# Performance work log

Measured on AMD Instinct MI355X. Metric: run time of the kernel, lower is better.

The kernel has to match this reference:

```python
import jax, jax.numpy as jnp
import numpy as np

EPS = 1e-5  # torch LayerNorm default


def _layer_norm(x, g, b):
    mu = jnp.mean(x, axis=-1, keepdims=True)
    var = jnp.mean(jnp.square(x - mu), axis=-1, keepdims=True)
    return (x - mu) * jax.lax.rsqrt(var + EPS) * g + b


def setup_inputs() -> dict:
    key = jax.random.key(0)
    ks = jax.random.split(key, 8)
    B, S, D = 4, 2048, 1024
    s = 1.0 / np.sqrt(D)
    return {
        "q": jax.random.normal(ks[0], (B, S, D), jnp.float32),
        "k": jax.random.normal(ks[1], (B, S, D), jnp.float32),
        "v": jax.random.normal(ks[2], (B, S, D), jnp.float32),
        "mask": jnp.ones((B, 1, S), jnp.int32),
        "Wq": jax.random.normal(ks[3], (D, D), jnp.float32) * s,
        "Wk": jax.random.normal(ks[4], (D, D), jnp.float32) * s,
        "Wv": jax.random.normal(ks[5], (D, D), jnp.float32) * s,
        "Wo": jax.random.normal(ks[6], (D, D), jnp.float32) * s,
        "ln_q_g": jnp.ones((D,), jnp.float32),
        "ln_q_b": jnp.zeros((D,), jnp.float32),
        "ln_k_g": jnp.ones((D,), jnp.float32),
        "ln_k_b": jnp.zeros((D,), jnp.float32),
        "ln_v_g": jnp.ones((D,), jnp.float32),
        "ln_v_b": jnp.zeros((D,), jnp.float32),
    }


def reference(q, k, v, mask, Wq, Wk, Wv, Wo,
              ln_q_g, ln_q_b, ln_k_g, ln_k_b, ln_v_g, ln_v_b):
    B, Lq, D = q.shape
    H = 16
    dk = D // H
    residual = q
    # pre-LN + bias-free projections
    qh = (_layer_norm(q, ln_q_g, ln_q_b) @ Wq).reshape(B, Lq, H, dk).transpose(0, 2, 1, 3)
    kh = (_layer_norm(k, ln_k_g, ln_k_b) @ Wk).reshape(B, -1, H, dk).transpose(0, 2, 1, 3)
    vh = (_layer_norm(v, ln_v_g, ln_v_b) @ Wv).reshape(B, -1, H, dk).transpose(0, 2, 1, 3)
    # scaled scores [B,H,Lq,Lk]
    scores = jnp.einsum('bhqd,bhkd->bhqk', qh, kh) / jnp.sqrt(jnp.float32(dk))
    pad = (mask == 0)[:, None, :, :]  # [B,1,*,Lk], True where masked
    scores = jnp.where(pad, -jnp.inf, scores)
    attn = jax.nn.softmax(scores, axis=-1)
    attn = jnp.where(pad, 0.0, attn)
    out = jnp.einsum('bhqk,bhkd->bhqd', attn, vh)
    out = out.transpose(0, 2, 1, 3).reshape(B, Lq, D)
    return out @ Wo + residual
```

## Files before the change

kernel.cpp:

```cpp
#include <hip/hip_runtime.h>
#include <stdint.h>

typedef __attribute__((ext_vector_type(8))) short short8;
typedef __attribute__((ext_vector_type(4))) float f32x4;
typedef __attribute__((ext_vector_type(4))) unsigned short us4;

#define B_ 4
#define S_ 2048
#define D_ 1024
#define H_ 16
#define DK_ 64

__device__ __forceinline__ unsigned short f2bf(float f) {
  union { float f; unsigned int u; } c; c.f = f;
  unsigned int r = (c.u + 0x7fffu + ((c.u >> 16) & 1u)) >> 16;
  return (unsigned short)r;
}

__device__ __forceinline__ unsigned int cvt_pk_bf16(float lo, float hi) {
  unsigned int r;
  asm("v_cvt_pk_bf16_f32 %0, %1, %2" : "=v"(r) : "v"(lo), "v"(hi));
  return r;
}

__device__ __forceinline__ float exp2_fast(float x) {
#if __has_builtin(__builtin_amdgcn_exp2f)
  return __builtin_amdgcn_exp2f(x);
#else
  float r; asm("v_exp_f32 %0, %1" : "=v"(r) : "v"(x)); return r;
#endif
}

__device__ __forceinline__ void glds16(const void* g, void* l) {
  __builtin_amdgcn_global_load_lds(
      (__attribute__((address_space(1))) void*)(uintptr_t)g,
      (__attribute__((address_space(3))) void*)l, 16, 0, 0);
}

__device__ __forceinline__ f32x4 mfma_bf16(short8 a, short8 b, f32x4 c) {
  return __builtin_amdgcn_mfma_f32_16x16x32_bf16(a, b, c, 0, 0, 0);
}

__global__ __launch_bounds__(256) void ln_bf16_3(const float* __restrict__ x0,
                                                 const float* __restrict__ x1,
                                                 const float* __restrict__ x2,
                                                 const float* __restrict__ g0,
                                                 const float* __restrict__ g1,
                                                 const float* __restrict__ g2,
                                                 const float* __restrict__ b0,
                                                 const float* __restrict__ b1,
                                                 const float* __restrict__ b2,
                                                 unsigned short* __restrict__ y0,
                                                 unsigned short* __restrict__ y1,
                                                 unsigned short* __restrict__ y2) {
  const int which = blockIdx.y;
  const float* x = which == 0 ? x0 : (which == 1 ? x1 : x2);
  const float* g = which == 0 ? g0 : (which == 1 ? g1 : g2);
  const float* bta = which == 0 ? b0 : (which == 1 ? b1 : b2);
  unsigned short* y = which == 0 ? y0 : (which == 1 ? y1 : y2);

  const int lane = threadIdx.x & 63, wid = threadIdx.x >> 6;
  const int row = blockIdx.x * 4 + wid;
  const float4* xr = (const float4*)(x + (size_t)row * D_);
  float4 v[4];
  float s1 = 0.f, s2 = 0.f;
#pragma unroll
  for (int i = 0; i < 4; ++i) {
    v[i] = xr[i * 64 + lane];
    s1 += v[i].x + v[i].y + v[i].z + v[i].w;
    s2 += v[i].x * v[i].x + v[i].y * v[i].y + v[i].z * v[i].z + v[i].w * v[i].w;
  }
#pragma unroll
  for (int m = 32; m; m >>= 1) { s1 += __shfl_xor(s1, m); s2 += __shfl_xor(s2, m); }
  const float mu = s1 * (1.f / D_);
  const float inv = rsqrtf(s2 * (1.f / D_) - mu * mu + 1e-5f);
  const float4* gp = (const float4*)g;
  const float4* bp = (const float4*)bta;
  us4* yr = (us4*)(y + (size_t)row * D_);
#pragma unroll
  for (int i = 0; i < 4; ++i) {
    float4 gv = gp[i * 64 + lane], bv = bp[i * 64 + lane];
    us4 o;
    o[0] = f2bf((v[i].x - mu) * inv * gv.x + bv.x);
    o[1] = f2bf((v[i].y - mu) * inv * gv.y + bv.y);
    o[2] = f2bf((v[i].z - mu) * inv * gv.z + bv.z);
    o[3] = f2bf((v[i].w - mu) * inv * gv.w + bv.w);
    yr[i * 64 + lane] = o;
  }
}

__global__ void wt_bf16_4(const float* __restrict__ W0, const float* __restrict__ W1,
                          const float* __restrict__ W2, const float* __restrict__ W3,
                          unsigned short* __restrict__ T0, unsigned short* __restrict__ T1,
                          unsigned short* __restrict__ T2, unsigned short* __restrict__ T3) {
  const int which = blockIdx.z;
  const float* W = which == 0 ? W0 : (which == 1 ? W1 : (which == 2 ? W2 : W3));
  unsigned short* Wt = which == 0 ? T0 : (which == 1 ? T1 : (which == 2 ? T2 : T3));
  __shared__ float t[32][33];
  const int n0 = blockIdx.x * 32, k0 = blockIdx.y * 32;
  const int tx = threadIdx.x, ty = threadIdx.y;
  for (int i = ty; i < 32; i += 8) t[i][tx] = W[(size_t)(k0 + i) * D_ + n0 + tx];
  __syncthreads();
  for (int i = ty; i < 32; i += 8)
    Wt[(size_t)(n0 + i) * D_ + k0 + tx] = f2bf(t[tx][i]);
}

__global__ __launch_bounds__(256, 2) void gemm_qkv(const unsigned short* __restrict__ Xq,
                                                   const unsigned short* __restrict__ Xk,
                                                   const unsigned short* __restrict__ Xv,
                                                   const unsigned short* __restrict__ Wq,
                                                   const unsigned short* __restrict__ Wk,
                                                   const unsigned short* __restrict__ Wv,
                                                   unsigned short* __restrict__ Qh,
                                                   unsigned short* __restrict__ Kh,
                                                   unsigned short* __restrict__ Vtb,
                                                   float qscale) {
  constexpr int K = D_;
  constexpr int NT = K / 64;
  __shared__ __attribute__((aligned(16))) unsigned short As[2][128][64];
  __shared__ __attribute__((aligned(16))) unsigned short Bs[2][128][64];
  const int z = blockIdx.z;
  const unsigned short* A = z == 0 ? Xq : (z == 1 ? Xk : Xv);
  const unsigned short* Bt = z == 0 ? Wq : (z == 1 ? Wk : Wv);
  const int tid = threadIdx.x;
  const int lane = tid & 63, wid = tid >> 6;
  const int lo16 = lane & 15, hi4 = lane >> 4;
  const int wr = wid >> 1, wc = wid & 1;
  const int gx = (int)gridDim.x;
  const int lid = (int)blockIdx.x + gx * (int)blockIdx.y;
  const int nwg = gx * (int)gridDim.y;
  const int swid = (lid & 7) * (nwg >> 3) + (lid >> 3);
  const int mbase = (swid / gx) * 128, nbase = (swid % gx) * 128;
  const int srow = lane >> 3, scol = (lane & 7) * 8;

  f32x4 acc[4][4] = {};

  auto stage = [&](int bufi, int kt) {
    const int kb = kt * 64;
#pragma unroll
    for (int c = 0; c < 4; ++c) {
      const int ch = wid * 4 + c;
      glds16(A + (size_t)(mbase + ch * 8 + srow) * K + kb + scol,
             (unsigned short*)&As[bufi][0][0] + ch * 512);
      glds16(Bt + (size_t)(nbase + ch * 8 + srow) * K + kb + scol,
             (unsigned short*)&Bs[bufi][0][0] + ch * 512);
    }
  };

  stage(0, 0);
  int cur = 0;

  for (int kt = 0; kt < NT; ++kt) {
    __syncthreads();
    if (kt + 1 < NT) stage(cur ^ 1, kt + 1);
    const unsigned short* Ap = &As[cur][0][0];
    const unsigned short* Bp = &Bs[cur][0][0];
    __builtin_amdgcn_s_setprio(1);
#pragma unroll
    for (int kk = 0; kk < 2; ++kk) {
      short8 af[4], bfr[4];
#pragma unroll
      for (int i = 0; i < 4; ++i)
        af[i] = *(const short8*)(Ap + (wr * 64 + i * 16 + lo16) * 64 + kk * 32 + hi4 * 8);
#pragma unroll
      for (int j = 0; j < 4; ++j)
        bfr[j] = *(const short8*)(Bp + (wc * 64 + j * 16 + lo16) * 64 + kk * 32 + hi4 * 8);
#pragma unroll
      for (int i = 0; i < 4; ++i)
#pragma unroll
        for (int j = 0; j < 4; ++j) acc[i][j] = mfma_bf16(af[i], bfr[j], acc[i][j]);
    }
    __builtin_amdgcn_s_setprio(0);
    cur ^= 1;
  }

  if (z < 2) {
    unsigned short* out = z == 0 ? Qh : Kh;
    const float scale = z == 0 ? qscale : 1.0f;
#pragma unroll
    for (int i = 0; i < 4; ++i) {
      const int row = mbase + wr * 64 + i * 16 + hi4 * 4;
      const int b = row >> 11, s = row & (S_ - 1);
#pragma unroll
      for (int j = 0; j < 4; ++j) {
        const int col = nbase + wc * 64 + j * 16 + lo16;
        const int h = col >> 6, d = col & 63;
        const size_t base = ((size_t)(b * H_ + h) * S_ + s) * DK_ + d;
#pragma unroll
        for (int r = 0; r < 4; ++r) out[base + (size_t)r * DK_] = f2bf(acc[i][j][r] * scale);
      }
    }
  } else {
#pragma unroll
    for (int i = 0; i < 4; ++i) {
      const int row = mbase + wr * 64 + i * 16 + hi4 * 4;
      const int b = row >> 11, s0 = row & (S_ - 1);
#pragma unroll
      for (int j = 0; j < 4; ++j) {
        const int col = nbase + wc * 64 + j * 16 + lo16;
        const int h = col >> 6, d = col & 63;
        us4 w;
#pragma unroll
        for (int r = 0; r < 4; ++r) w[r] = f2bf(acc[i][j][r]);
        *(us4*)(Vtb + ((size_t)(b * H_ + h) * DK_ + d) * S_ + s0) = w;
      }
    }
  }
}

__global__ __launch_bounds__(256, 2) void gemm_out(const unsigned short* __restrict__ A,
                                                   const unsigned short* __restrict__ Bt,
                                                   float* __restrict__ out,
                                                   const float* __restrict__ resid) {
  constexpr int K = D_;
  constexpr int NT = K / 64;
  __shared__ __attribute__((aligned(16))) unsigned short As[2][128][64];
  __shared__ __attribute__((aligned(16))) unsigned short Bs[2][128][64];
  const int tid = threadIdx.x;
  const int lane = tid & 63, wid = tid >> 6;
  const int lo16 = lane & 15, hi4 = lane >> 4;
  const int wr = wid >> 1, wc = wid & 1;
  const int gx = (int)gridDim.x;
  const int lid = (int)blockIdx.x + gx * (int)blockIdx.y;
  const int nwg = gx * (int)gridDim.y;
  const int swid = (lid & 7) * (nwg >> 3) + (lid >> 3);
  const int mbase = (swid / gx) * 128, nbase = (swid % gx) * 128;
  const int srow = lane >> 3, scol = (lane & 7) * 8;

  f32x4 acc[4][4] = {};

  auto stage = [&](int bufi, int kt) {
    const int kb = kt * 64;
#pragma unroll
    for (int c = 0; c < 4; ++c) {
      const int ch = wid * 4 + c;
      glds16(A + (size_t)(mbase + ch * 8 + srow) * K + kb + scol,
             (unsigned short*)&As[bufi][0][0] + ch * 512);
      glds16(Bt + (size_t)(nbase + ch * 8 + srow) * K + kb + scol,
             (unsigned short*)&Bs[bufi][0][0] + ch * 512);
    }
  };

  stage(0, 0);
  int cur = 0;

  for (int kt = 0; kt < NT; ++kt) {
    __syncthreads();
    if (kt + 1 < NT) stage(cur ^ 1, kt + 1);
    const unsigned short* Ap = &As[cur][0][0];
    const unsigned short* Bp = &Bs[cur][0][0];
    __builtin_amdgcn_s_setprio(1);
#pragma unroll
    for (int kk = 0; kk < 2; ++kk) {
      short8 af[4], bfr[4];
#pragma unroll
      for (int i = 0; i < 4; ++i)
        af[i] = *(const short8*)(Ap + (wr * 64 + i * 16 + lo16) * 64 + kk * 32 + hi4 * 8);
#pragma unroll
      for (int j = 0; j < 4; ++j)
        bfr[j] = *(const short8*)(Bp + (wc * 64 + j * 16 + lo16) * 64 + kk * 32 + hi4 * 8);
#pragma unroll
      for (int i = 0; i < 4; ++i)
#pragma unroll
        for (int j = 0; j < 4; ++j) acc[i][j] = mfma_bf16(af[i], bfr[j], acc[i][j]);
    }
    __builtin_amdgcn_s_setprio(0);
    cur ^= 1;
  }

#pragma unroll
  for (int i = 0; i < 4; ++i) {
    const int row = mbase + wr * 64 + i * 16 + hi4 * 4;
#pragma unroll
    for (int j = 0; j < 4; ++j) {
      const int col = nbase + wc * 64 + j * 16 + lo16;
      const size_t idx = (size_t)row * D_ + col;
#pragma unroll
      for (int r = 0; r < 4; ++r)
        out[idx + (size_t)r * D_] = acc[i][j][r] + resid[idx + (size_t)r * D_];
    }
  }
}

__global__ __launch_bounds__(512, 2) void attn_k(const unsigned short* __restrict__ Qh,
                                                 const unsigned short* __restrict__ Kh,
                                                 const unsigned short* __restrict__ Vt,
                                                 const int* __restrict__ mask,
                                                 unsigned short* __restrict__ O) {
  __shared__ __attribute__((aligned(16))) unsigned short Ks[2][64][64];
  __shared__ __attribute__((aligned(16))) unsigned short Vs[2][64][64];
  __shared__ __attribute__((aligned(16))) unsigned short Ps[256][72];
  __shared__ unsigned short MskL[S_];
  __shared__ unsigned char TileOk[S_ / 64];
  const int tid = threadIdx.x, lane = tid & 63, wid = tid >> 6;
  const int lo16 = lane & 15, hi4 = lane >> 4;
  const int swz = (lo16 & 7) << 3;
  const int lid = (int)blockIdx.x + 8 * (int)blockIdx.y;
  const int swid = (lid & 7) * 64 + (lid >> 3);
  const int qb = swid & 7, bh = swid >> 3;
  const int b = bh >> 4, h = bh & 15;
  const unsigned short* Qb = Qh + (size_t)bh * S_ * DK_;
  const unsigned short* Kb = Kh + (size_t)bh * S_ * DK_;
  const unsigned short* Vb = Vt + (size_t)bh * DK_ * S_;
  const int* mb = mask + b * S_;
  const int srow = lane >> 3;
  const int scolx = ((lane & 7) ^ srow) * 8;

  for (int t = tid; t < S_; t += 512) MskL[t] = (unsigned short)(mb[t] != 0);
  __syncthreads();
  if (tid < S_ / 64) {
    int ok = 1;
    for (int j = 0; j < 64; ++j) ok &= (int)MskL[tid * 64 + j];
    TileOk[tid] = (unsigned char)ok;
  }

  short8 qf[2][2];
#pragma unroll
  for (int i = 0; i < 2; ++i)
#pragma unroll
    for (int kk = 0; kk < 2; ++kk)
      qf[i][kk] = *(const short8*)(Qb + (size_t)(qb * 256 + wid * 32 + i * 16 + lo16) * DK_ +
                                   kk * 32 + hi4 * 8);

  f32x4 o[2][4] = {};
  float lsum0 = 0.f, lsum1 = 0.f;

  auto stageKV = [&](int bufi, int kt) {
    glds16(Kb + (size_t)(kt * 64 + wid * 8 + srow) * DK_ + scolx,
           (unsigned short*)&Ks[bufi][0][0] + wid * 512);
    glds16(Vb + (size_t)(wid * 8 + srow) * S_ + kt * 64 + scolx,
           (unsigned short*)&Vs[bufi][0][0] + wid * 512);
  };

  auto tile = [&](int bufc, int kt) {
    __syncthreads();
    if (kt + 1 < S_ / 64) stageKV(bufc ^ 1, kt + 1);

    const unsigned short* Kc = &Ks[bufc][0][0];
    const int tok = (int)TileOk[kt];
    short8 kf[2][4];
#pragma unroll
    for (int kk = 0; kk < 2; ++kk)
#pragma unroll
      for (int nf = 0; nf < 4; ++nf)
        kf[kk][nf] = *(const short8*)(Kc + (nf * 16 + lo16) * 64 + ((kk * 32 + hi4 * 8) ^ swz));
#pragma unroll
    for (int i = 0; i < 2; ++i) {
      f32x4 p[4] = {};
      __builtin_amdgcn_s_setprio(1);
#pragma unroll
      for (int kk = 0; kk < 2; ++kk)
#pragma unroll
        for (int nf = 0; nf < 4; ++nf) p[nf] = mfma_bf16(kf[kk][nf], qf[i][kk], p[nf]);
      __builtin_amdgcn_s_setprio(0);
      if (!tok) {
#pragma unroll
        for (int nf = 0; nf < 4; ++nf) {
          const us4 mk = *(const us4*)&MskL[kt * 64 + nf * 16 + hi4 * 4];
#pragma unroll
          for (int r = 0; r < 4; ++r)
            if (!mk[r]) p[nf][r] = -1e30f;
        }
      }
      const int prow = wid * 32 + i * 16 + lo16;
      float ls = 0.f;
#pragma unroll
      for (int nf = 0; nf < 4; ++nf) {
        float e0 = exp2_fast(p[nf][0]);
        float e1 = exp2_fast(p[nf][1]);
        float e2 = exp2_fast(p[nf][2]);
        float e3 = exp2_fast(p[nf][3]);
        ls += (e0 + e1) + (e2 + e3);
        uint2 w;
        w.x = cvt_pk_bf16(e0, e1);
        w.y = cvt_pk_bf16(e2, e3);
        *(uint2*)&Ps[prow][nf * 16 + hi4 * 4] = w;
      }
      if (i == 0) lsum0 += ls; else lsum1 += ls;
    }
    const unsigned short* Vc = &Vs[bufc][0][0];
    __builtin_amdgcn_s_setprio(1);
#pragma unroll
    for (int kk = 0; kk < 2; ++kk) {
      const int pc = kk * 32 + hi4 * 8;
      short8 pa0 = *(const short8*)&Ps[wid * 32 + 0 + lo16][pc];
      short8 pa1 = *(const short8*)&Ps[wid * 32 + 16 + lo16][pc];
#pragma unroll
      for (int df = 0; df < 4; ++df) {
        short8 vf = *(const short8*)(Vc + (df * 16 + lo16) * 64 + (pc ^ swz));
        o[0][df] = mfma_bf16(pa0, vf, o[0][df]);
        o[1][df] = mfma_bf16(pa1, vf, o[1][df]);
      }
    }
    __builtin_amdgcn_s_setprio(0);
  };

  stageKV(0, 0);
#pragma unroll 1
  for (int kt = 0; kt < S_ / 64; kt += 2) {
    tile(0, kt);
    tile(1, kt + 1);
  }

  lsum0 += __shfl_xor(lsum0, 16); lsum0 += __shfl_xor(lsum0, 32);
  lsum1 += __shfl_xor(lsum1, 16); lsum1 += __shfl_xor(lsum1, 32);
#pragma unroll
  for (int i = 0; i < 2; ++i) {
#pragma unroll
    for (int r = 0; r < 4; ++r) {
      const int ql = hi4 * 4 + r;
      const float l = __shfl(i == 0 ? lsum0 : lsum1, ql);
      const float rl = l > 0.f ? 1.f / l : 0.f;
      const int srowg = qb * 256 + wid * 32 + i * 16 + ql;
      const size_t base = ((size_t)b * S_ + srowg) * D_ + h * 64;
#pragma unroll
      for (int df = 0; df < 4; ++df) O[base + df * 16 + lo16] = f2bf(o[i][df][r] * rl);
    }
  }
}

extern "C" void kernel_launch(void* const* d_in, const int* in_sizes, int n_in,
                              void* d_out, int out_size, void* d_ws, size_t ws_size,
                              hipStream_t stream) {
  const float* q = (const float*)d_in[0];
  const float* k = (const float*)d_in[1];
  const float* v = (const float*)d_in[2];
  const int* mask = (const int*)d_in[3];
  const float* Wq = (const float*)d_in[4];
  const float* Wk = (const float*)d_in[5];
  const float* Wv = (const float*)d_in[6];
  const float* Wo = (const float*)d_in[7];
  const float* lnqg = (const float*)d_in[8];
  const float* lnqb = (const float*)d_in[9];
  const float* lnkg = (const float*)d_in[10];
  const float* lnkb = (const float*)d_in[11];
  const float* lnvg = (const float*)d_in[12];
  const float* lnvb = (const float*)d_in[13];

  uint8_t* ws = (uint8_t*)d_ws;
  const size_t MB = 1024ull * 1024ull;
  unsigned short* Xq = (unsigned short*)(ws + 0 * MB);
  unsigned short* Xk = (unsigned short*)(ws + 16 * MB);
  unsigned short* Xv = (unsigned short*)(ws + 32 * MB);
  unsigned short* Wqt = (unsigned short*)(ws + 48 * MB);
  unsigned short* Wkt = (unsigned short*)(ws + 50 * MB);
  unsigned short* Wvt = (unsigned short*)(ws + 52 * MB);
  unsigned short* Wot = (unsigned short*)(ws + 54 * MB);
  unsigned short* Qh = (unsigned short*)(ws + 56 * MB);
  unsigned short* Kh = (unsigned short*)(ws + 72 * MB);
  unsigned short* Vtb = Xq;
  unsigned short* Ob = Xk;

  hipLaunchKernelGGL(wt_bf16_4, dim3(32, 32, 4), dim3(32, 8), 0, stream,
                     Wq, Wk, Wv, Wo, Wqt, Wkt, Wvt, Wot);

  hipLaunchKernelGGL(ln_bf16_3, dim3(2048, 3), dim3(256), 0, stream,
                     q, k, v, lnqg, lnkg, lnvg, lnqb, lnkb, lnvb, Xq, Xk, Xv);

  const float qscale = 0.125f * 1.4426950408889634f;
  hipLaunchKernelGGL(gemm_qkv, dim3(D_ / 128, (B_ * S_) / 128, 3), dim3(256), 0, stream,
                     Xq, Xk, Xv, Wqt, Wkt, Wvt, Qh, Kh, Vtb, qscale);

  hipLaunchKernelGGL(attn_k, dim3(S_ / 256, B_ * H_), dim3(512), 0, stream, Qh, Kh, Vtb, mask, Ob);

  hipLaunchKernelGGL(gemm_out, dim3(D_ / 128, (B_ * S_) / 128), dim3(256), 0, stream,
                     Ob, Wot, (float*)d_out, q);
}
```

Baseline: 237.6 us.

## Swizzle P tile in LDS, reload K fragments per MFMA, loop with buffer toggle

Drops the padding on the P staging buffer in shared memory and uses an XOR swizzle for P writes and reads, which shrinks LDS use and is meant to avoid bank conflicts. K fragments are now loaded from LDS next to each MFMA instead of all being preloaded, which lowers register pressure. The two-tile unrolled lambda becomes a plain loop with a toggled buffer index. An explicit lgkmcnt wait and a sched_barrier are added before the PV stage. The P store and load index rows differently (prow vs wid*32+lo16), but both rows share the same lo16, so the swizzle stays consistent. Reloading K once per row group doubles K LDS reads and may expose latency.

```diff
diff --git a/kernel.cpp b/kernel.cpp
--- a/kernel.cpp
+++ b/kernel.cpp
@@ -289,7 +289,7 @@
                                                  unsigned short* __restrict__ O) {
   __shared__ __attribute__((aligned(16))) unsigned short Ks[2][64][64];
   __shared__ __attribute__((aligned(16))) unsigned short Vs[2][64][64];
-  __shared__ __attribute__((aligned(16))) unsigned short Ps[256][72];
+  __shared__ __attribute__((aligned(16))) unsigned short Ps[256][64];
   __shared__ unsigned short MskL[S_];
   __shared__ unsigned char TileOk[S_ / 64];
   const int tid = threadIdx.x, lane = tid & 63, wid = tid >> 6;
@@ -332,18 +332,15 @@
            (unsigned short*)&Vs[bufi][0][0] + wid * 512);
   };
 
-  auto tile = [&](int bufc, int kt) {
+  stageKV(0, 0);
+  int cur = 0;
+
+  for (int kt = 0; kt < S_ / 64; ++kt) {
     __syncthreads();
-    if (kt + 1 < S_ / 64) stageKV(bufc ^ 1, kt + 1);
-
-    const unsigned short* Kc = &Ks[bufc][0][0];
+    if (kt + 1 < S_ / 64) stageKV(cur ^ 1, kt + 1);
+
+    const unsigned short* Kc = &Ks[cur][0][0];
     const int tok = (int)TileOk[kt];
-    short8 kf[2][4];
-#pragma unroll
-    for (int kk = 0; kk < 2; ++kk)
-#pragma unroll
-      for (int nf = 0; nf < 4; ++nf)
-        kf[kk][nf] = *(const short8*)(Kc + (nf * 16 + lo16) * 64 + ((kk * 32 + hi4 * 8) ^ swz));
 #pragma unroll
     for (int i = 0; i < 2; ++i) {
       f32x4 p[4] = {};
@@ -351,7 +348,10 @@
 #pragma unroll
       for (int kk = 0; kk < 2; ++kk)
 #pragma unroll
-        for (int nf = 0; nf < 4; ++nf) p[nf] = mfma_bf16(kf[kk][nf], qf[i][kk], p[nf]);
+        for (int nf = 0; nf < 4; ++nf) {
+          short8 kf = *(const short8*)(Kc + (nf * 16 + lo16) * 64 + ((kk * 32 + hi4 * 8) ^ swz));
+          p[nf] = mfma_bf16(kf, qf[i][kk], p[nf]);
+        }
       __builtin_amdgcn_s_setprio(0);
       if (!tok) {
 #pragma unroll
@@ -374,32 +374,28 @@
         uint2 w;
         w.x = cvt_pk_bf16(e0, e1);
         w.y = cvt_pk_bf16(e2, e3);
-        *(uint2*)&Ps[prow][nf * 16 + hi4 * 4] = w;
+        *(uint2*)&Ps[prow][(nf * 16 + hi4 * 4) ^ swz] = w;
       }
       if (i == 0) lsum0 += ls; else lsum1 += ls;
     }
-    const unsigned short* Vc = &Vs[bufc][0][0];
+    asm volatile("s_waitcnt lgkmcnt(0)" ::: "memory");
+    __builtin_amdgcn_sched_barrier(0);
+    const unsigned short* Vc = &Vs[cur][0][0];
     __builtin_amdgcn_s_setprio(1);
 #pragma unroll
     for (int kk = 0; kk < 2; ++kk) {
-      const int pc = kk * 32 + hi4 * 8;
-      short8 pa0 = *(const short8*)&Ps[wid * 32 + 0 + lo16][pc];
-      short8 pa1 = *(const short8*)&Ps[wid * 32 + 16 + lo16][pc];
+      const int pc = (kk * 32 + hi4 * 8) ^ swz;
+      short8 pa0 = *(const short8*)((const unsigned short*)Ps + (wid * 32 + 0 + lo16) * 64 + pc);
+      short8 pa1 = *(const short8*)((const unsigned short*)Ps + (wid * 32 + 16 + lo16) * 64 + pc);
 #pragma unroll
       for (int df = 0; df < 4; ++df) {
-        short8 vf = *(const short8*)(Vc + (df * 16 + lo16) * 64 + (pc ^ swz));
+        short8 vf = *(const short8*)(Vc + (df * 16 + lo16) * 64 + pc);
         o[0][df] = mfma_bf16(pa0, vf, o[0][df]);
         o[1][df] = mfma_bf16(pa1, vf, o[1][df]);
       }
     }
     __builtin_amdgcn_s_setprio(0);
-  };
-
-  stageKV(0, 0);
-#pragma unroll 1
-  for (int kt = 0; kt < S_ / 64; kt += 2) {
-    tile(0, kt);
-    tile(1, kt + 1);
+    cur ^= 1;
   }
 
   lsum0 += __shfl_xor(lsum0, 16); lsum0 += __shfl_xor(lsum0, 32);
```

Result: faster. 219.3 us (-7.7%).
